# Optimization experiments

Hardware: AMD Instinct MI355X
Metric: run time of the kernel (lower is better)

## Reference

```python
import jax, jax.numpy as jnp
import numpy as np

NUM_FREQS = 10
EPS = 1e-6


def _posenc(x):
    # NeRF positional encoding with identity: [x, sin(2^i x), cos(2^i x)]
    freqs = 2.0 ** jnp.arange(NUM_FREQS, dtype=x.dtype)  # [L]
    xb = x[..., None, :] * freqs[:, None]                # [..., L, D]
    four = jnp.sin(jnp.concatenate([xb, xb + 0.5 * jnp.pi], axis=-2))
    return jnp.concatenate([x, four.reshape(*x.shape[:-1], -1)], axis=-1)


def _ln(x, s, b):
    mu = jnp.mean(x, axis=-1, keepdims=True)
    var = jnp.mean(jnp.square(x - mu), axis=-1, keepdims=True)
    return (x - mu) * jax.lax.rsqrt(var + EPS) * s + b


def _layer(net, chunk, hW, hb, hls, hlb, wW, wb, bW, bb_, ls, lb):
    # hyper net (hyper_depth=1): Dense -> LayerNorm -> relu
    h = jax.nn.relu(_ln(chunk @ hW + hb, hls, hlb))
    n_in = net.shape[-1]
    n_out = bb_.shape[-1]
    # generate per-point weight matrix [K,P,N,M] and bias [K,P,N]
    w = (h @ wW + wb).reshape(*h.shape[:-1], n_out, n_in)
    b = h @ bW + bb_
    net = jnp.einsum('kpm,kpnm->kpn', net, w) + b
    return jax.nn.relu(_ln(net, ls, lb))


def _forward(rays, latent_tokens, token_embeddings, h_W0, h_b0, h_ln_s0, h_ln_b0,
             w_W0, w_b0, bb_W0, bb_b0, ln_s0, ln_b0,
             h_W, h_b, h_ln_s, h_ln_b, w_W, w_b, bb_W, bb_b, ln_s, ln_b,
             rgb_W, rgb_b):
    origins = rays[..., 0:3]
    dirs = rays[..., 3:6]
    plucker = jnp.concatenate([dirs, jnp.cross(origins, dirs)], axis=-1)  # [K,P,6]
    net = _posenc(plucker)  # [K,P,126]

    K, T, Z = latent_tokens.shape
    emb = jnp.broadcast_to(token_embeddings[None], (K, T, token_embeddings.shape[-1]))
    lt = jnp.concatenate([latent_tokens, emb], axis=-1).reshape(K, 1, -1)  # [K,1,T*(Z+E)]
    P = rays.shape[1]
    latent = jnp.broadcast_to(lt, (K, P, lt.shape[-1]))
    skips = jnp.split(latent, 8, axis=-1)  # 8 chunks of [K,P,128]

    net = _layer(net, skips[0], h_W0, h_b0, h_ln_s0, h_ln_b0,
                 w_W0, w_b0, bb_W0, bb_b0, ln_s0, ln_b0)
    for i in range(7):
        net = _layer(net, skips[i + 1], h_W[i], h_b[i], h_ln_s[i], h_ln_b[i],
                     w_W[i], w_b[i], bb_W[i], bb_b[i], ln_s[i], ln_b[i])
    return jax.nn.sigmoid(net @ rgb_W + rgb_b)


def setup_inputs() -> dict:
    key = jax.random.key(0)
    ks = jax.random.split(key, 12)
    K, P, T, Z, W = 2, 4096, 8, 64, 64
    IN0 = 6 * (1 + 2 * NUM_FREQS)  # 126
    f32 = jnp.float32
    d = {}
    d['rays'] = jax.random.normal(ks[0], (K, P, 6), f32)
    d['latent_tokens'] = jax.random.normal(ks[1], (K, T, Z), f32)
    d['token_embeddings'] = jax.random.normal(ks[2], (T, 64), f32)
    # layer 0 (input dim 126)
    d['h_W0'] = jax.random.normal(ks[3], (Z + 64, W), f32)
    d['h_b0'] = jnp.zeros((W,), f32)
    d['h_ln_s0'] = jnp.ones((W,), f32)
    d['h_ln_b0'] = jnp.zeros((W,), f32)
    d['w_W0'] = jax.random.normal(ks[4], (W, IN0 * W), f32)
    d['w_b0'] = jnp.zeros((IN0 * W,), f32)
    d['bb_W0'] = jax.random.normal(ks[5], (W, W), f32)
    d['bb_b0'] = jnp.zeros((W,), f32)
    d['ln_s0'] = jnp.ones((W,), f32)
    d['ln_b0'] = jnp.zeros((W,), f32)
    # layers 1..7 (input dim 64), stacked
    L = 7
    d['h_W'] = jax.random.normal(ks[6], (L, Z + 64, W), f32)
    d['h_b'] = jnp.zeros((L, W), f32)
    d['h_ln_s'] = jnp.ones((L, W), f32)
    d['h_ln_b'] = jnp.zeros((L, W), f32)
    d['w_W'] = jax.random.normal(ks[7], (L, W, W * W), f32)
    d['w_b'] = jnp.zeros((L, W * W), f32)
    d['bb_W'] = jax.random.normal(ks[8], (L, W, W), f32)
    d['bb_b'] = jnp.zeros((L, W), f32)
    d['ln_s'] = jnp.ones((L, W), f32)
    d['ln_b'] = jnp.zeros((L, W), f32)
    d['rgb_W'] = jax.random.normal(ks[9], (W, 3), f32)
    d['rgb_b'] = jnp.zeros((3,), f32)
    return d


def reference(rays, latent_tokens, token_embeddings, h_W0, h_b0, h_ln_s0, h_ln_b0,
              w_W0, w_b0, bb_W0, bb_b0, ln_s0, ln_b0,
              h_W, h_b, h_ln_s, h_ln_b, w_W, w_b, bb_W, bb_b, ln_s, ln_b,
              rgb_W, rgb_b):
    return _forward(rays, latent_tokens, token_embeddings, h_W0, h_b0, h_ln_s0, h_ln_b0,
                    w_W0, w_b0, bb_W0, bb_b0, ln_s0, ln_b0,
                    h_W, h_b, h_ln_s, h_ln_b, w_W, w_b, bb_W, bb_b, ln_s, ln_b,
                    rgb_W, rgb_b)
```

## Files before the change

### kernel.cpp

```cpp
#include <hip/hip_runtime.h>
#include <math.h>

#define EPSF 1e-6f
typedef unsigned int uint;
typedef _Float16 f16x2 __attribute__((ext_vector_type(2)));
typedef __fp16 h16x2 __attribute__((ext_vector_type(2)));

__device__ __forceinline__ uint rlu(uint v, int srclane) {
    return (uint)__builtin_amdgcn_readlane((int)v, srclane);
}

__device__ __forceinline__ float dot2u(uint w, uint a, float c) {
#if __has_builtin(__builtin_amdgcn_fdot2)
    return __builtin_amdgcn_fdot2(__builtin_bit_cast(f16x2, w),
                                  __builtin_bit_cast(f16x2, a), c, false);
#else
    f16x2 wv = __builtin_bit_cast(f16x2, w), av = __builtin_bit_cast(f16x2, a);
    return c + (float)wv.x * (float)wv.x + (float)wv.y * (float)av.y;
#endif
}

__device__ __forceinline__ uint pkact(float lo, float hi) {
#if __has_builtin(__builtin_amdgcn_cvt_pkrtz)
    h16x2 p = __builtin_amdgcn_cvt_pkrtz(lo, hi);
    return __builtin_bit_cast(uint, p);
#else
    f16x2 p; p.x = (_Float16)lo; p.y = (_Float16)hi;
    return __builtin_bit_cast(uint, p);
#endif
}

__device__ __forceinline__ float bpermf(int byteaddr, float v) {
    return __int_as_float(__builtin_amdgcn_ds_bpermute(byteaddr, __float_as_int(v)));
}

__device__ __forceinline__ void ln_stats(float a, float& mu, float& rstd) {
    float s1 = a, s2 = a * a;
#pragma unroll
    for (int off = 32; off > 0; off >>= 1) {
        s1 += __shfl_xor(s1, off, 64);
        s2 += __shfl_xor(s2, off, 64);
    }
    mu = s1 * (1.0f / 64.0f);
    float var = fmaxf(s2 * (1.0f / 64.0f) - mu * mu, 0.0f);
    rstd = rsqrtf(var + EPSF);
}

__device__ __forceinline__ float wave_sum64(float v) {
#pragma unroll
    for (int off = 32; off > 0; off >>= 1) v += __shfl_xor(v, off, 64);
    return v;
}

__device__ __forceinline__ float posenc_elem(const float* pl, int e) {
    if (e < 6) return pl[e];
    int t = e - 6;
    int j = t / 6;
    int i = t - j * 6;
    int jm = (j < 10) ? j : (j - 10);
    float arg = pl[i] * (float)(1 << jm);
    if (j >= 10) arg += 1.5707963705062866f;
    return sinf(arg);
}

__global__ __launch_bounds__(128) void precompute_kernel(
    const float* __restrict__ latent_tokens, const float* __restrict__ token_embeddings,
    const float* __restrict__ h_W0, const float* __restrict__ h_b0,
    const float* __restrict__ h_ln_s0, const float* __restrict__ h_ln_b0,
    const float* __restrict__ w_W0, const float* __restrict__ w_b0,
    const float* __restrict__ bb_W0, const float* __restrict__ bb_b0,
    const float* __restrict__ h_W, const float* __restrict__ h_b,
    const float* __restrict__ h_ln_s, const float* __restrict__ h_ln_b,
    const float* __restrict__ w_W, const float* __restrict__ w_b,
    const float* __restrict__ bb_W, const float* __restrict__ bb_b,
    float* __restrict__ ws, int offBbytes)
{
    const int s = blockIdx.x;
    const int l = blockIdx.y;
    const int tid = threadIdx.x;
    const int lane = tid & 63;
    const int warp = tid >> 6;

    __shared__ float s_chunk[2][128];
    __shared__ float s_h[2][64];

#pragma unroll
    for (int t = tid; t < 256; t += 128) {
        int k = t >> 7, m = t & 127;
        s_chunk[k][m] = (m < 64) ? latent_tokens[(k * 8 + l) * 64 + m]
                                 : token_embeddings[l * 64 + (m - 64)];
    }
    __syncthreads();

    const float* hW  = (l == 0) ? h_W0    : h_W    + (size_t)(l - 1) * 128 * 64;
    const float* hb  = (l == 0) ? h_b0    : h_b    + (l - 1) * 64;
    const float* hls = (l == 0) ? h_ln_s0 : h_ln_s + (l - 1) * 64;
    const float* hlb = (l == 0) ? h_ln_b0 : h_ln_b + (l - 1) * 64;

    {
        float a = hb[lane];
#pragma unroll 16
        for (int m = 0; m < 128; m++) a += s_chunk[warp][m] * hW[m * 64 + lane];
        float mu, rstd;
        ln_stats(a, mu, rstd);
        s_h[warp][lane] = fmaxf((a - mu) * rstd * hls[lane] + hlb[lane], 0.0f);
    }
    __syncthreads();

    const int n_in  = (l == 0) ? 126 : 64;
    const int nflat = 64 * n_in;
    const int slice = nflat / 32;
    const float* wW = (l == 0) ? w_W0 : w_W + (size_t)(l - 1) * 64 * 4096;
    const float* wb = (l == 0) ? w_b0 : w_b + (size_t)(l - 1) * 4096;
    _Float16* wsH = (_Float16*)ws;

    for (int o = s * slice + tid; o < s * slice + slice; o += 128) {
        float wbv = wb[o];
        float a0 = wbv, a1 = wbv;
#pragma unroll 16
        for (int j = 0; j < 64; j++) {
            float w = wW[(size_t)j * nflat + o];
            a0 += s_h[0][j] * w;
            a1 += s_h[1][j] * w;
        }
        int n = o / n_in, m = o - n * n_in;
        if (l == 0) {
            wsH[n * 128 + m]        = (_Float16)a0;
            wsH[8192 + n * 128 + m] = (_Float16)a1;
        } else {
            _Float16* b0p = wsH + 16384 + (size_t)(l - 1) * 4096;
            b0p[n * 64 + m]            = (_Float16)a0;
            b0p[7 * 4096 + n * 64 + m] = (_Float16)a1;
        }
    }

    if (l == 0 && s == 0) {
        int n = tid >> 1, c = tid & 1;
        wsH[n * 128 + 126 + c] = (_Float16)0.0f;
        wsH[8192 + n * 128 + 126 + c] = (_Float16)0.0f;
    }

    if (s == 0) {
        const float* bW  = (l == 0) ? bb_W0 : bb_W + (size_t)(l - 1) * 64 * 64;
        const float* bb_ = (l == 0) ? bb_b0 : bb_b + (l - 1) * 64;
        float a = bb_[lane];
#pragma unroll 16
        for (int j = 0; j < 64; j++) a += s_h[warp][j] * bW[j * 64 + lane];
        ((float*)((char*)ws + offBbytes))[(warp * 8 + l) * 64 + lane] = a;
    }
}

#define MC1(wc, pp) \
    accq0 = dot2u(wc, rlu(pk0, (pp)), accq0); \
    accq1 = dot2u(wc, rlu(pk1, (pp)), accq1); \
    accq2 = dot2u(wc, rlu(pk2, (pp)), accq2); \
    accq3 = dot2u(wc, rlu(pk3, (pp)), accq3);
#define MACCH(W, P0) { uint4 _w = (W); MC1(_w.x, (P0)) MC1(_w.y, (P0)+1) MC1(_w.z, (P0)+2) MC1(_w.w, (P0)+3) }
#define MACLAYER_A  MACCH(A0,0) MACCH(A1,4) MACCH(A2,8)  MACCH(A3,12) MACCH(A4,16) MACCH(A5,20) MACCH(A6,24) MACCH(A7,28)
#define MACLAYER_B  MACCH(B0,0) MACCH(B1,4) MACCH(B2,8)  MACCH(B3,12) MACCH(B4,16) MACCH(B5,20) MACCH(B6,24) MACCH(B7,28)
#define MACLAYER_B32 MACCH(B0,32) MACCH(B1,36) MACCH(B2,40) MACCH(B3,44) MACCH(B4,48) MACCH(B5,52) MACCH(B6,56) MACCH(B7,60)
#define LOAD_A(p) A0=(p)[0]; A1=(p)[1]; A2=(p)[2]; A3=(p)[3]; A4=(p)[4]; A5=(p)[5]; A6=(p)[6]; A7=(p)[7];
#define LOAD_B(p) B0=(p)[0]; B1=(p)[1]; B2=(p)[2]; B3=(p)[3]; B4=(p)[4]; B5=(p)[5]; B6=(p)[6]; B7=(p)[7];
#define BIAS(v)  accq0=(v); accq1=(v); accq2=(v); accq3=(v);
#define LNQ(aq, pq, S, B) { float mu, rstd; ln_stats(aq, mu, rstd); \
    aq = fmaxf((aq - mu) * rstd * (S) + (B), 0.0f); \
    pq = pkact(bpermf(pa0, aq), bpermf(pa1, aq)); }
#define LNP(S, B) LNQ(accq0, pk0, S, B) LNQ(accq1, pk1, S, B) LNQ(accq2, pk2, S, B) LNQ(accq3, pk3, S, B)

__global__ __launch_bounds__(256, 2) void forward_kernel(
    const float* __restrict__ rays,
    const float* __restrict__ ln_s0, const float* __restrict__ ln_b0,
    const float* __restrict__ ln_s, const float* __restrict__ ln_b,
    const float* __restrict__ rgb_W, const float* __restrict__ rgb_b,
    const float* __restrict__ ws, int offBbytes,
    float* __restrict__ out, int K, int P)
{
    const int warp = threadIdx.x >> 6;
    const int lane = threadIdx.x & 63;
    const int total = K * P;
    const int r0 = (blockIdx.x * 4 + warp) * 4;
    if (r0 >= total) return;
    const int k = r0 / P;

    const char* wsB = (const char*)ws;
    const uint4* row0 = (const uint4*)(wsB + (size_t)k * 16384 + lane * 256);
    const uint4* rowL = (const uint4*)(wsB + 32768 + (size_t)k * 57344 + lane * 128);
    const float* beff = (const float*)(wsB + offBbytes) + k * 512;

    uint4 A0,A1,A2,A3,A4,A5,A6,A7, B0,B1,B2,B3,B4,B5,B6,B7;
    LOAD_A(row0); LOAD_B(row0 + 8);

    float be[8];
#pragma unroll
    for (int i = 0; i < 8; i++) be[i] = beff[i * 64 + lane];
    float s0v = ln_s0[lane], b0v = ln_b0[lane];
    float sl[7], bl[7];
#pragma unroll
    for (int i = 0; i < 7; i++) { sl[i] = ln_s[i * 64 + lane]; bl[i] = ln_b[i * 64 + lane]; }

    const int pa0 = ((2 * lane) & 63) << 2;
    const int pa1 = ((2 * lane + 1) & 63) << 2;

    uint pk0, pk1, pk2, pk3;
    {
        const int e0 = 2 * lane, e1 = 2 * lane + 1;
#pragma unroll
        for (int q = 0; q < 4; q++) {
            int r = r0 + q; if (r > total - 1) r = total - 1;
            float o0 = rays[r * 6 + 0], o1 = rays[r * 6 + 1], o2 = rays[r * 6 + 2];
            float d0 = rays[r * 6 + 3], d1 = rays[r * 6 + 4], d2 = rays[r * 6 + 5];
            float pl[6];
            pl[0] = d0; pl[1] = d1; pl[2] = d2;
            pl[3] = o1 * d2 - o2 * d1;
            pl[4] = o2 * d0 - o0 * d2;
            pl[5] = o0 * d1 - o1 * d0;
            float v0 = (e0 < 126) ? posenc_elem(pl, e0) : 0.0f;
            float v1 = (e1 < 126) ? posenc_elem(pl, e1) : 0.0f;
            uint p = pkact(v0, v1);
            if (q == 0) pk0 = p; else if (q == 1) pk1 = p; else if (q == 2) pk2 = p; else pk3 = p;
        }
    }

    float accq0, accq1, accq2, accq3;

    BIAS(be[0]);
    MACLAYER_A;
    LOAD_A(rowL);
    MACLAYER_B32;
    LNP(s0v, b0v);

    BIAS(be[1]); MACLAYER_A; LOAD_B(rowL + 512);  LNP(sl[0], bl[0]);
    BIAS(be[2]); MACLAYER_B; LOAD_A(rowL + 1024); LNP(sl[1], bl[1]);
    BIAS(be[3]); MACLAYER_A; LOAD_B(rowL + 1536); LNP(sl[2], bl[2]);
    BIAS(be[4]); MACLAYER_B; LOAD_A(rowL + 2048); LNP(sl[3], bl[3]);
    BIAS(be[5]); MACLAYER_A; LOAD_B(rowL + 2560); LNP(sl[4], bl[4]);
    BIAS(be[6]); MACLAYER_B; LOAD_A(rowL + 3072); LNP(sl[5], bl[5]);
    BIAS(be[7]); MACLAYER_A;                      LNP(sl[6], bl[6]);

    float w0 = rgb_W[lane * 3 + 0], w1 = rgb_W[lane * 3 + 1], w2 = rgb_W[lane * 3 + 2];
    float b0 = rgb_b[0], b1 = rgb_b[1], b2 = rgb_b[2];
#pragma unroll
    for (int q = 0; q < 4; q++) {
        float a = (q == 0) ? accq0 : (q == 1) ? accq1 : (q == 2) ? accq2 : accq3;
        float c0 = wave_sum64(a * w0);
        float c1 = wave_sum64(a * w1);
        float c2 = wave_sum64(a * w2);
        if (lane == 0 && r0 + q < total) {
            out[(r0 + q) * 3 + 0] = 1.0f / (1.0f + expf(-(c0 + b0)));
            out[(r0 + q) * 3 + 1] = 1.0f / (1.0f + expf(-(c1 + b1)));
            out[(r0 + q) * 3 + 2] = 1.0f / (1.0f + expf(-(c2 + b2)));
        }
    }
}

extern "C" void kernel_launch(void* const* d_in, const int* in_sizes, int n_in,
                              void* d_out, int out_size, void* d_ws, size_t ws_size,
                              hipStream_t stream) {
    const float* rays    = (const float*)d_in[0];
    const float* latent  = (const float*)d_in[1];
    const float* tok_emb = (const float*)d_in[2];
    const float* h_W0    = (const float*)d_in[3];
    const float* h_b0    = (const float*)d_in[4];
    const float* h_ln_s0 = (const float*)d_in[5];
    const float* h_ln_b0 = (const float*)d_in[6];
    const float* w_W0    = (const float*)d_in[7];
    const float* w_b0    = (const float*)d_in[8];
    const float* bb_W0   = (const float*)d_in[9];
    const float* bb_b0   = (const float*)d_in[10];
    const float* ln_s0   = (const float*)d_in[11];
    const float* ln_b0   = (const float*)d_in[12];
    const float* h_W     = (const float*)d_in[13];
    const float* h_b     = (const float*)d_in[14];
    const float* h_ln_s  = (const float*)d_in[15];
    const float* h_ln_b  = (const float*)d_in[16];
    const float* w_W     = (const float*)d_in[17];
    const float* w_b     = (const float*)d_in[18];
    const float* bb_W    = (const float*)d_in[19];
    const float* bb_b    = (const float*)d_in[20];
    const float* ln_s    = (const float*)d_in[21];
    const float* ln_b    = (const float*)d_in[22];
    const float* rgb_W   = (const float*)d_in[23];
    const float* rgb_b   = (const float*)d_in[24];
    float* out = (float*)d_out;

    const int K = in_sizes[1] / (8 * 64);
    const int P = in_sizes[0] / (6 * K);
    const int offBbytes = K * 16384 + K * 7 * 8192;

    float* ws = (float*)d_ws;

    dim3 pgrid(32, 8);
    precompute_kernel<<<pgrid, 128, 0, stream>>>(
        latent, tok_emb, h_W0, h_b0, h_ln_s0, h_ln_b0, w_W0, w_b0, bb_W0, bb_b0,
        h_W, h_b, h_ln_s, h_ln_b, w_W, w_b, bb_W, bb_b, ws, offBbytes);

    const int total = K * P;
    const int blocks = (total + 15) / 16;
    forward_kernel<<<blocks, 256, 0, stream>>>(
        rays, ln_s0, ln_b0, ln_s, ln_b, rgb_W, rgb_b,
        ws, offBbytes, out, K, P);
}
```

Measured before the change: 143.0 us.

## Replace per-lane fdot2 readlane MACs with 16x16x32 f16 MFMA tiles

Rewrites the forward kernel so each 64-thread block handles 16 rays and computes every layer's 64-wide matmul with MFMA 16x16x32 f16 instructions. Activations are staged in shared memory as f16 A fragments, and the next layer's weights are double-buffered in registers. LayerNorm reductions now run over 16-lane groups. This targets the scalar readlane/fdot2 bottleneck, at the cost of an LDS round-trip per layer and smaller blocks.

```diff
diff --git a/kernel.cpp b/kernel.cpp
--- a/kernel.cpp
+++ b/kernel.cpp
@@ -3,22 +3,10 @@
 
 #define EPSF 1e-6f
 typedef unsigned int uint;
+typedef _Float16 f16x8v __attribute__((ext_vector_type(8)));
+typedef float f32x4v __attribute__((ext_vector_type(4)));
 typedef _Float16 f16x2 __attribute__((ext_vector_type(2)));
 typedef __fp16 h16x2 __attribute__((ext_vector_type(2)));
-
-__device__ __forceinline__ uint rlu(uint v, int srclane) {
-    return (uint)__builtin_amdgcn_readlane((int)v, srclane);
-}
-
-__device__ __forceinline__ float dot2u(uint w, uint a, float c) {
-#if __has_builtin(__builtin_amdgcn_fdot2)
-    return __builtin_amdgcn_fdot2(__builtin_bit_cast(f16x2, w),
-                                  __builtin_bit_cast(f16x2, a), c, false);
-#else
-    f16x2 wv = __builtin_bit_cast(f16x2, w), av = __builtin_bit_cast(f16x2, a);
-    return c + (float)wv.x * (float)wv.x + (float)wv.y * (float)av.y;
-#endif
-}
 
 __device__ __forceinline__ uint pkact(float lo, float hi) {
 #if __has_builtin(__builtin_amdgcn_cvt_pkrtz)
@@ -30,8 +18,17 @@
 #endif
 }
 
-__device__ __forceinline__ float bpermf(int byteaddr, float v) {
-    return __int_as_float(__builtin_amdgcn_ds_bpermute(byteaddr, __float_as_int(v)));
+__device__ __forceinline__ f32x4v mfma16(uint4 a, uint4 b, f32x4v c) {
+    return __builtin_amdgcn_mfma_f32_16x16x32_f16(
+        __builtin_bit_cast(f16x8v, a), __builtin_bit_cast(f16x8v, b), c, 0, 0, 0);
+}
+
+__device__ __forceinline__ void red16_2(float& x, float& y) {
+#pragma unroll
+    for (int off = 1; off < 16; off <<= 1) {
+        x += __shfl_xor(x, off, 64);
+        y += __shfl_xor(y, off, 64);
+    }
 }
 
 __device__ __forceinline__ void ln_stats(float a, float& mu, float& rstd) {
@@ -44,12 +41,6 @@
     mu = s1 * (1.0f / 64.0f);
     float var = fmaxf(s2 * (1.0f / 64.0f) - mu * mu, 0.0f);
     rstd = rsqrtf(var + EPSF);
-}
-
-__device__ __forceinline__ float wave_sum64(float v) {
-#pragma unroll
-    for (int off = 32; off > 0; off >>= 1) v += __shfl_xor(v, off, 64);
-    return v;
 }
 
 __device__ __forceinline__ float posenc_elem(const float* pl, int e) {
@@ -150,24 +141,7 @@
     }
 }
 
-#define MC1(wc, pp) \
-    accq0 = dot2u(wc, rlu(pk0, (pp)), accq0); \
-    accq1 = dot2u(wc, rlu(pk1, (pp)), accq1); \
-    accq2 = dot2u(wc, rlu(pk2, (pp)), accq2); \
-    accq3 = dot2u(wc, rlu(pk3, (pp)), accq3);
-#define MACCH(W, P0) { uint4 _w = (W); MC1(_w.x, (P0)) MC1(_w.y, (P0)+1) MC1(_w.z, (P0)+2) MC1(_w.w, (P0)+3) }
-#define MACLAYER_A  MACCH(A0,0) MACCH(A1,4) MACCH(A2,8)  MACCH(A3,12) MACCH(A4,16) MACCH(A5,20) MACCH(A6,24) MACCH(A7,28)
-#define MACLAYER_B  MACCH(B0,0) MACCH(B1,4) MACCH(B2,8)  MACCH(B3,12) MACCH(B4,16) MACCH(B5,20) MACCH(B6,24) MACCH(B7,28)
-#define MACLAYER_B32 MACCH(B0,32) MACCH(B1,36) MACCH(B2,40) MACCH(B3,44) MACCH(B4,48) MACCH(B5,52) MACCH(B6,56) MACCH(B7,60)
-#define LOAD_A(p) A0=(p)[0]; A1=(p)[1]; A2=(p)[2]; A3=(p)[3]; A4=(p)[4]; A5=(p)[5]; A6=(p)[6]; A7=(p)[7];
-#define LOAD_B(p) B0=(p)[0]; B1=(p)[1]; B2=(p)[2]; B3=(p)[3]; B4=(p)[4]; B5=(p)[5]; B6=(p)[6]; B7=(p)[7];
-#define BIAS(v)  accq0=(v); accq1=(v); accq2=(v); accq3=(v);
-#define LNQ(aq, pq, S, B) { float mu, rstd; ln_stats(aq, mu, rstd); \
-    aq = fmaxf((aq - mu) * rstd * (S) + (B), 0.0f); \
-    pq = pkact(bpermf(pa0, aq), bpermf(pa1, aq)); }
-#define LNP(S, B) LNQ(accq0, pk0, S, B) LNQ(accq1, pk1, S, B) LNQ(accq2, pk2, S, B) LNQ(accq3, pk3, S, B)
-
-__global__ __launch_bounds__(256, 2) void forward_kernel(
+__global__ __launch_bounds__(64) void forward_kernel(
     const float* __restrict__ rays,
     const float* __restrict__ ln_s0, const float* __restrict__ ln_b0,
     const float* __restrict__ ln_s, const float* __restrict__ ln_b,
@@ -175,80 +149,169 @@
     const float* __restrict__ ws, int offBbytes,
     float* __restrict__ out, int K, int P)
 {
-    const int warp = threadIdx.x >> 6;
-    const int lane = threadIdx.x & 63;
+    __shared__ _Float16 acts[16 * 136];
+    const int lane = threadIdx.x;
+    const int quad = lane >> 4;
+    const int c    = lane & 15;
     const int total = K * P;
-    const int r0 = (blockIdx.x * 4 + warp) * 4;
+    const int r0 = blockIdx.x * 16;
     if (r0 >= total) return;
     const int k = r0 / P;
 
-    const char* wsB = (const char*)ws;
-    const uint4* row0 = (const uint4*)(wsB + (size_t)k * 16384 + lane * 256);
-    const uint4* rowL = (const uint4*)(wsB + 32768 + (size_t)k * 57344 + lane * 128);
-    const float* beff = (const float*)(wsB + offBbytes) + k * 512;
-
-    uint4 A0,A1,A2,A3,A4,A5,A6,A7, B0,B1,B2,B3,B4,B5,B6,B7;
-    LOAD_A(row0); LOAD_B(row0 + 8);
-
-    float be[8];
-#pragma unroll
-    for (int i = 0; i < 8; i++) be[i] = beff[i * 64 + lane];
-    float s0v = ln_s0[lane], b0v = ln_b0[lane];
-    float sl[7], bl[7];
-#pragma unroll
-    for (int i = 0; i < 7; i++) { sl[i] = ln_s[i * 64 + lane]; bl[i] = ln_b[i * 64 + lane]; }
-
-    const int pa0 = ((2 * lane) & 63) << 2;
-    const int pa1 = ((2 * lane + 1) & 63) << 2;
-
-    uint pk0, pk1, pk2, pk3;
+    const _Float16* W0 = (const _Float16*)ws + (size_t)k * 8192;
+    const _Float16* WL = (const _Float16*)ws + 16384 + (size_t)k * 28672;
+    const float* beff = (const float*)((const char*)ws + offBbytes) + k * 512;
+
+    uint4 B0f[4][4];
+#pragma unroll
+    for (int t = 0; t < 4; t++)
+#pragma unroll
+        for (int kc = 0; kc < 4; kc++)
+            B0f[t][kc] = *(const uint4*)(W0 + (t * 16 + c) * 128 + kc * 32 + quad * 8);
+
     {
-        const int e0 = 2 * lane, e1 = 2 * lane + 1;
-#pragma unroll
-        for (int q = 0; q < 4; q++) {
-            int r = r0 + q; if (r > total - 1) r = total - 1;
-            float o0 = rays[r * 6 + 0], o1 = rays[r * 6 + 1], o2 = rays[r * 6 + 2];
-            float d0 = rays[r * 6 + 3], d1 = rays[r * 6 + 4], d2 = rays[r * 6 + 5];
-            float pl[6];
-            pl[0] = d0; pl[1] = d1; pl[2] = d2;
-            pl[3] = o1 * d2 - o2 * d1;
-            pl[4] = o2 * d0 - o0 * d2;
-            pl[5] = o0 * d1 - o1 * d0;
-            float v0 = (e0 < 126) ? posenc_elem(pl, e0) : 0.0f;
-            float v1 = (e1 < 126) ? posenc_elem(pl, e1) : 0.0f;
-            uint p = pkact(v0, v1);
-            if (q == 0) pk0 = p; else if (q == 1) pk1 = p; else if (q == 2) pk2 = p; else pk3 = p;
-        }
-    }
-
-    float accq0, accq1, accq2, accq3;
-
-    BIAS(be[0]);
-    MACLAYER_A;
-    LOAD_A(rowL);
-    MACLAYER_B32;
-    LNP(s0v, b0v);
-
-    BIAS(be[1]); MACLAYER_A; LOAD_B(rowL + 512);  LNP(sl[0], bl[0]);
-    BIAS(be[2]); MACLAYER_B; LOAD_A(rowL + 1024); LNP(sl[1], bl[1]);
-    BIAS(be[3]); MACLAYER_A; LOAD_B(rowL + 1536); LNP(sl[2], bl[2]);
-    BIAS(be[4]); MACLAYER_B; LOAD_A(rowL + 2048); LNP(sl[3], bl[3]);
-    BIAS(be[5]); MACLAYER_A; LOAD_B(rowL + 2560); LNP(sl[4], bl[4]);
-    BIAS(be[6]); MACLAYER_B; LOAD_A(rowL + 3072); LNP(sl[5], bl[5]);
-    BIAS(be[7]); MACLAYER_A;                      LNP(sl[6], bl[6]);
-
-    float w0 = rgb_W[lane * 3 + 0], w1 = rgb_W[lane * 3 + 1], w2 = rgb_W[lane * 3 + 2];
-    float b0 = rgb_b[0], b1 = rgb_b[1], b2 = rgb_b[2];
-#pragma unroll
-    for (int q = 0; q < 4; q++) {
-        float a = (q == 0) ? accq0 : (q == 1) ? accq1 : (q == 2) ? accq2 : accq3;
-        float c0 = wave_sum64(a * w0);
-        float c1 = wave_sum64(a * w1);
-        float c2 = wave_sum64(a * w2);
-        if (lane == 0 && r0 + q < total) {
-            out[(r0 + q) * 3 + 0] = 1.0f / (1.0f + expf(-(c0 + b0)));
-            out[(r0 + q) * 3 + 1] = 1.0f / (1.0f + expf(-(c1 + b1)));
-            out[(r0 + q) * 3 + 2] = 1.0f / (1.0f + expf(-(c2 + b2)));
+        int rr = lane >> 2;
+        int r = r0 + rr; if (r > total - 1) r = total - 1;
+        float o0 = rays[r * 6 + 0], o1 = rays[r * 6 + 1], o2 = rays[r * 6 + 2];
+        float d0 = rays[r * 6 + 3], d1 = rays[r * 6 + 4], d2 = rays[r * 6 + 5];
+        float pl[6];
+        pl[0] = d0; pl[1] = d1; pl[2] = d2;
+        pl[3] = o1 * d2 - o2 * d1;
+        pl[4] = o2 * d0 - o0 * d2;
+        pl[5] = o0 * d1 - o1 * d0;
+        int e0 = (lane & 3) * 32;
+        uint pk[16];
+#pragma unroll
+        for (int i = 0; i < 16; i++) {
+            int ea = e0 + 2 * i;
+            float va = (ea < 126) ? posenc_elem(pl, ea) : 0.0f;
+            float vb = (ea + 1 < 126) ? posenc_elem(pl, ea + 1) : 0.0f;
+            pk[i] = pkact(va, vb);
+        }
+        uint4* dst = (uint4*)(acts + rr * 136 + e0);
+#pragma unroll
+        for (int i = 0; i < 4; i++)
+            dst[i] = make_uint4(pk[4 * i], pk[4 * i + 1], pk[4 * i + 2], pk[4 * i + 3]);
+    }
+
+    uint4 Bf[2][4][2];
+#pragma unroll
+    for (int t = 0; t < 4; t++)
+#pragma unroll
+        for (int kc = 0; kc < 2; kc++)
+            Bf[1][t][kc] = *(const uint4*)(WL + (t * 16 + c) * 64 + kc * 32 + quad * 8);
+
+    float ga[4], be_[4];
+    f32x4v C[4];
+#pragma unroll
+    for (int t = 0; t < 4; t++) {
+        int n = t * 16 + c;
+        ga[t] = ln_s0[n]; be_[t] = ln_b0[n];
+        float bv = beff[n];
+        C[t] = (f32x4v){bv, bv, bv, bv};
+    }
+
+    {
+        uint4 A0[4];
+#pragma unroll
+        for (int kc = 0; kc < 4; kc++)
+            A0[kc] = *(const uint4*)(acts + c * 136 + kc * 32 + quad * 8);
+#pragma unroll
+        for (int t = 0; t < 4; t++)
+#pragma unroll
+            for (int kc = 0; kc < 4; kc++)
+                C[t] = mfma16(A0[kc], B0f[t][kc], C[t]);
+    }
+
+    float alast[4][4];
+
+#pragma unroll
+    for (int e = 0; e < 4; e++) {
+        float s1 = C[0][e] + C[1][e] + C[2][e] + C[3][e];
+        float s2 = C[0][e]*C[0][e] + C[1][e]*C[1][e] + C[2][e]*C[2][e] + C[3][e]*C[3][e];
+        red16_2(s1, s2);
+        float mu = s1 * (1.0f / 64.0f);
+        float var = fmaxf(s2 * (1.0f / 64.0f) - mu * mu, 0.0f);
+        float rstd = rsqrtf(var + EPSF);
+        int row = quad * 4 + e;
+#pragma unroll
+        for (int t = 0; t < 4; t++) {
+            float a = fmaxf((C[t][e] - mu) * rstd * ga[t] + be_[t], 0.0f);
+            acts[row * 136 + t * 16 + c] = (_Float16)a;
+        }
+    }
+
+#pragma unroll
+    for (int l = 1; l < 8; l++) {
+        uint4 A[2];
+        A[0] = *(const uint4*)(acts + c * 136 + quad * 8);
+        A[1] = *(const uint4*)(acts + c * 136 + 32 + quad * 8);
+        if (l < 7) {
+            const _Float16* Wn = WL + (size_t)l * 4096;
+#pragma unroll
+            for (int t = 0; t < 4; t++)
+#pragma unroll
+                for (int kc = 0; kc < 2; kc++)
+                    Bf[(l + 1) & 1][t][kc] = *(const uint4*)(Wn + (t * 16 + c) * 64 + kc * 32 + quad * 8);
+        }
+        float g2[4], b2[4];
+#pragma unroll
+        for (int t = 0; t < 4; t++) {
+            int n = t * 16 + c;
+            g2[t] = ln_s[(l - 1) * 64 + n];
+            b2[t] = ln_b[(l - 1) * 64 + n];
+            float bv = beff[l * 64 + n];
+            C[t] = (f32x4v){bv, bv, bv, bv};
+        }
+#pragma unroll
+        for (int t = 0; t < 4; t++)
+#pragma unroll
+            for (int kc = 0; kc < 2; kc++)
+                C[t] = mfma16(A[kc], Bf[l & 1][t][kc], C[t]);
+
+#pragma unroll
+        for (int e = 0; e < 4; e++) {
+            float s1 = C[0][e] + C[1][e] + C[2][e] + C[3][e];
+            float s2 = C[0][e]*C[0][e] + C[1][e]*C[1][e] + C[2][e]*C[2][e] + C[3][e]*C[3][e];
+            red16_2(s1, s2);
+            float mu = s1 * (1.0f / 64.0f);
+            float var = fmaxf(s2 * (1.0f / 64.0f) - mu * mu, 0.0f);
+            float rstd = rsqrtf(var + EPSF);
+            int row = quad * 4 + e;
+#pragma unroll
+            for (int t = 0; t < 4; t++) {
+                float a = fmaxf((C[t][e] - mu) * rstd * g2[t] + b2[t], 0.0f);
+                if (l < 7) acts[row * 136 + t * 16 + c] = (_Float16)a;
+                else       alast[t][e] = a;
+            }
+        }
+    }
+
+    float w0_[4], w1_[4], w2_[4];
+#pragma unroll
+    for (int t = 0; t < 4; t++) {
+        int n = t * 16 + c;
+        w0_[t] = rgb_W[n * 3 + 0];
+        w1_[t] = rgb_W[n * 3 + 1];
+        w2_[t] = rgb_W[n * 3 + 2];
+    }
+    float rb0 = rgb_b[0], rb1 = rgb_b[1], rb2 = rgb_b[2];
+#pragma unroll
+    for (int e = 0; e < 4; e++) {
+        float p0 = alast[0][e]*w0_[0] + alast[1][e]*w0_[1] + alast[2][e]*w0_[2] + alast[3][e]*w0_[3];
+        float p1 = alast[0][e]*w1_[0] + alast[1][e]*w1_[1] + alast[2][e]*w1_[2] + alast[3][e]*w1_[3];
+        float p2 = alast[0][e]*w2_[0] + alast[1][e]*w2_[1] + alast[2][e]*w2_[2] + alast[3][e]*w2_[3];
+#pragma unroll
+        for (int off = 1; off < 16; off <<= 1) {
+            p0 += __shfl_xor(p0, off, 64);
+            p1 += __shfl_xor(p1, off, 64);
+            p2 += __shfl_xor(p2, off, 64);
+        }
+        int r = r0 + quad * 4 + e;
+        if (c < 3 && r < total) {
+            float p  = (c == 0) ? p0 : (c == 1) ? p1 : p2;
+            float bb = (c == 0) ? rb0 : (c == 1) ? rb1 : rb2;
+            out[r * 3 + c] = 1.0f / (1.0f + expf(-(p + bb)));
         }
     }
 }
@@ -296,7 +359,7 @@
 
     const int total = K * P;
     const int blocks = (total + 15) / 16;
-    forward_kernel<<<blocks, 256, 0, stream>>>(
+    forward_kernel<<<blocks, 64, 0, stream>>>(
         rays, ln_s0, ln_b0, ln_s, ln_b, rgb_W, rgb_b,
         ws, offBbytes, out, K, P);
 }
```

Measured after the change: 132.5 us. 7.3% less time.
